# Performance work log

Hardware: AMD Instinct MI355X
Metric: run time of the kernel (lower is better)

Reference implementation:

```python
import math
import jax, jax.numpy as jnp
import numpy as np

D_MODEL = 1024
NHEAD = 16
DK = D_MODEL // NHEAD
FACTOR = 5
B, L = 4, 8192
U = max(1, min(FACTOR * math.ceil(math.log(L + 1)), L))  # 50


def setup_inputs() -> dict:
    key = jax.random.key(0)
    ks = jax.random.split(key, 10)
    s = 1.0 / math.sqrt(D_MODEL)
    inp = {
        "x": jax.random.normal(ks[0], (B, L, D_MODEL), dtype=jnp.float32),
        "Wq": jax.random.normal(ks[1], (D_MODEL, D_MODEL), dtype=jnp.float32) * s,
        "bq": jnp.zeros((D_MODEL,), dtype=jnp.float32),
        "Wk": jax.random.normal(ks[2], (D_MODEL, D_MODEL), dtype=jnp.float32) * s,
        "bk": jnp.zeros((D_MODEL,), dtype=jnp.float32),
        "Wv": jax.random.normal(ks[3], (D_MODEL, D_MODEL), dtype=jnp.float32) * s,
        "bv": jnp.zeros((D_MODEL,), dtype=jnp.float32),
        "Wo": jax.random.normal(ks[4], (D_MODEL, D_MODEL), dtype=jnp.float32) * s,
        "bo": jnp.zeros((D_MODEL,), dtype=jnp.float32),
        # randperm(L)[:U] sample of key positions (constant, like torch.randperm)
        "idx_k": jax.random.permutation(ks[5], L)[:U].astype(jnp.int32),
    }
    return inp


def reference(x, Wq, bq, Wk, bk, Wv, bv, Wo, bo, idx_k):
    Bv, Lv, _ = x.shape
    H, dk = NHEAD, DK
    u = idx_k.shape[0]
    scale = 1.0 / math.sqrt(dk)

    # projections -> [B, H, L, dk]
    Q = (x @ Wq.T + bq).reshape(Bv, Lv, H, dk).transpose(0, 2, 1, 3)
    K = (x @ Wk.T + bk).reshape(Bv, Lv, H, dk).transpose(0, 2, 1, 3)
    V = (x @ Wv.T + bv).reshape(Bv, Lv, H, dk).transpose(0, 2, 1, 3)

    # sampled scores against u random keys: [B, H, L, u]
    K_samp = K[:, :, idx_k, :]
    scores = jnp.einsum("bhld,bhud->bhlu", Q, K_samp) * scale
    M = scores.max(-1) - scores.mean(-1)                 # [B, H, L]
    _, top_idx = jax.lax.top_k(M, u)                      # [B, H, u]

    # gather selected queries and attend against ALL keys
    Q_top = jnp.take_along_axis(Q, top_idx[..., None], axis=2)   # [B, H, u, dk]
    attn = jax.nn.softmax(jnp.einsum("bhud,bhld->bhul", Q_top, K) * scale, axis=-1)
    ctx_top = jnp.einsum("bhul,bhld->bhud", attn, V)              # [B, H, u, dk]

    # mean(V) fallback, scatter selected contexts back
    ctx = jnp.broadcast_to(V.mean(axis=2, keepdims=True), (Bv, H, Lv, dk))
    bidx = jnp.arange(Bv)[:, None, None]
    hidx = jnp.arange(H)[None, :, None]
    ctx = ctx.at[bidx, hidx, top_idx].set(ctx_top)

    ctx = ctx.transpose(0, 2, 1, 3).reshape(Bv, Lv, H * dk)
    return ctx @ Wo.T + bo
```

## Files before the change

kernel.cpp:

```cpp
#include <hip/hip_runtime.h>
#include <hip/hip_bf16.h>

#define B_ 4
#define L_ 8192
#define D_ 1024
#define H_ 16
#define SCALE 0.125f
#define NC 8
#define QPAD 64
#define RS 72

typedef __attribute__((ext_vector_type(8))) short bf16x8;
typedef __attribute__((ext_vector_type(4))) float f32x4;

__device__ __forceinline__ void gl2lds16(const void* g, void* s) {
    __builtin_amdgcn_global_load_lds(
        (const __attribute__((address_space(1))) unsigned int*)g,
        (__attribute__((address_space(3))) unsigned int*)s, 16, 0, 0);
}

__device__ __forceinline__ unsigned short bfbits(float a) {
    __hip_bfloat16 h = __float2bfloat16(a);
    return *(unsigned short*)&h;
}
__device__ __forceinline__ float bf2f(unsigned short u) {
    return __uint_as_float(((unsigned)u) << 16);
}

__global__ __launch_bounds__(256) void split3_kernel(const float* __restrict__ in,
        unsigned short* __restrict__ ph, unsigned short* __restrict__ pm,
        unsigned short* __restrict__ pl, int n4) {
    int i = blockIdx.x * 256 + threadIdx.x;
    if (i >= n4) return;
    float4 v = ((const float4*)in)[i];
    float c[4] = {v.x, v.y, v.z, v.w};
    unsigned short h[4], m[4], l[4];
    #pragma unroll
    for (int j = 0; j < 4; ++j) {
        float a = c[j];
        unsigned short hb = bfbits(a);
        float rh = a - bf2f(hb);
        unsigned short mb = bfbits(rh);
        float rm = rh - bf2f(mb);
        h[j] = hb; m[j] = mb; l[j] = bfbits(rm);
    }
    ((ushort4*)ph)[i] = *(ushort4*)h;
    ((ushort4*)pm)[i] = *(ushort4*)m;
    ((ushort4*)pl)[i] = *(ushort4*)l;
}

__global__ __launch_bounds__(256) void split2_kernel(const float* __restrict__ in,
        unsigned short* __restrict__ ph, unsigned short* __restrict__ pm, int n4) {
    int i = blockIdx.x * 256 + threadIdx.x;
    if (i >= n4) return;
    float4 v = ((const float4*)in)[i];
    float c[4] = {v.x, v.y, v.z, v.w};
    unsigned short h[4], m[4];
    #pragma unroll
    for (int j = 0; j < 4; ++j) {
        float a = c[j];
        unsigned short hb = bfbits(a);
        float rh = a - bf2f(hb);
        h[j] = hb; m[j] = bfbits(rh);
    }
    ((ushort4*)ph)[i] = *(ushort4*)h;
    ((ushort4*)pm)[i] = *(ushort4*)m;
}

__global__ __launch_bounds__(256) void xmean_kernel(const float* __restrict__ x,
                                                    float* __restrict__ xmean) {
    int c = blockIdx.x;
    int j = blockIdx.y * 256 + threadIdx.x;
    int b = blockIdx.z;
    const float* xp = x + ((size_t)b * L_ + (size_t)c * 256) * D_ + j;
    float s = 0.f;
    for (int l = 0; l < 256; ++l) s += xp[(size_t)l * D_];
    atomicAdd(&xmean[b * D_ + j], s * (1.0f / L_));
}

__global__ __launch_bounds__(256) void vecmat_kernel(const float* __restrict__ in,
                                                     const float* __restrict__ W,
                                                     const float* __restrict__ bias,
                                                     float* __restrict__ out) {
    __shared__ float vs[D_];
    int b = blockIdx.y;
    int j = blockIdx.x * 256 + threadIdx.x;
    for (int t = threadIdx.x; t < D_; t += 256) vs[t] = in[b * D_ + t];
    __syncthreads();
    const float* wr = W + (size_t)j * D_;
    float acc = 0.f;
    #pragma unroll 4
    for (int k = 0; k < D_; k += 4) {
        float4 w4 = *(const float4*)(wr + k);
        acc += vs[k] * w4.x + vs[k + 1] * w4.y + vs[k + 2] * w4.z + vs[k + 3] * w4.w;
    }
    out[b * D_ + j] = acc + bias[j];
}

__global__ __launch_bounds__(256) void ksamp_kernel(const float* __restrict__ x,
                                                    const float* __restrict__ Wk,
                                                    const float* __restrict__ bk,
                                                    const int* __restrict__ idx_k,
                                                    float* __restrict__ Ksamp, int U) {
    __shared__ float vs[D_];
    int u = blockIdx.x, b = blockIdx.y;
    int row = idx_k[u];
    const float* xp = x + ((size_t)b * L_ + row) * D_;
    for (int t = threadIdx.x; t < D_; t += 256) vs[t] = xp[t];
    __syncthreads();
    #pragma unroll
    for (int r = 0; r < 4; ++r) {
        int j = r * 256 + threadIdx.x;
        const float* wr = Wk + (size_t)j * D_;
        float acc = 0.f;
        #pragma unroll 4
        for (int k = 0; k < D_; k += 4) {
            float4 w4 = *(const float4*)(wr + k);
            acc += vs[k] * w4.x + vs[k + 1] * w4.y + vs[k + 2] * w4.z + vs[k + 3] * w4.w;
        }
        Ksamp[((size_t)b * U + u) * D_ + j] = acc + bk[j];
    }
}

#define TM 128
#define TN 128
#define BK 32
#define TSZ (TM * BK)

__global__ __launch_bounds__(256) void qkv_mfma_q(
    const unsigned short* __restrict__ xh, const unsigned short* __restrict__ xm,
    const unsigned short* __restrict__ xl,
    const unsigned short* __restrict__ qh, const unsigned short* __restrict__ qm,
    const unsigned short* __restrict__ ql,
    const float* __restrict__ bq, float* __restrict__ Q) {
    __shared__ __align__(16) unsigned short As[3][TSZ];
    __shared__ __align__(16) unsigned short Bs[3][TSZ];

    const int f  = blockIdx.y * 8 + blockIdx.x;
    const int w  = (f & 7) * 256 + (f >> 3);
    const int n0 = (w & 7) * TN;
    const int m0 = (w >> 3) * TM;
    const int tid = threadIdx.x;

    const int srow = tid >> 2;
    const int scol = (tid & 3) * 8;

    const int wave = tid >> 6;
    const int lane = tid & 63;
    const int wm = (wave & 1) * 64;
    const int wn = (wave >> 1) * 64;
    const int fr = lane & 15;
    const int fk = (lane >> 4) * 8;
    const int rbase = (lane >> 4) * 4;

    f32x4 acc[4][4];
    #pragma unroll
    for (int i = 0; i < 4; ++i)
        #pragma unroll
        for (int j = 0; j < 4; ++j)
            acc[i][j] = (f32x4){0.f, 0.f, 0.f, 0.f};

    const size_t aBase = (size_t)(m0 + srow) * D_ + scol;
    const size_t bBase = (size_t)(n0 + srow) * D_ + scol;

    bf16x8 af[4], bfv[4];
    auto loadA = [&](const unsigned short* t) {
        #pragma unroll
        for (int i = 0; i < 4; ++i)
            af[i] = *(const bf16x8*)(t + (wm + i * 16 + fr) * BK + fk);
    };
    auto loadB = [&](const unsigned short* t) {
        #pragma unroll
        for (int j = 0; j < 4; ++j)
            bfv[j] = *(const bf16x8*)(t + (wn + j * 16 + fr) * BK + fk);
    };
    auto prod = [&]() {
        #pragma unroll
        for (int i = 0; i < 4; ++i)
            #pragma unroll
            for (int j = 0; j < 4; ++j)
                acc[i][j] = __builtin_amdgcn_mfma_f32_16x16x32_bf16(
                    af[i], bfv[j], acc[i][j], 0, 0, 0);
    };
    auto stage = [&](const unsigned short* g, unsigned short* s, int kt, size_t base) {
        gl2lds16(g + base + kt, s + tid * 8);
        gl2lds16(g + base + (size_t)64 * D_ + kt, s + tid * 8 + 2048);
    };

    for (int kt = 0; kt < D_; kt += BK) {
        stage(xh, &As[0][0], kt, aBase);
        stage(xm, &As[1][0], kt, aBase);
        stage(xl, &As[2][0], kt, aBase);
        stage(qh, &Bs[0][0], kt, bBase);
        stage(qm, &Bs[1][0], kt, bBase);
        stage(ql, &Bs[2][0], kt, bBase);
        __syncthreads();
        loadA(&As[0][0]); loadB(&Bs[0][0]); prod();
        loadB(&Bs[1][0]); prod();
        loadB(&Bs[2][0]); prod();
        loadA(&As[1][0]); loadB(&Bs[0][0]); prod();
        loadB(&Bs[1][0]); prod();
        loadA(&As[2][0]); loadB(&Bs[0][0]); prod();
        __syncthreads();
    }

    float biasv[4];
    #pragma unroll
    for (int j = 0; j < 4; ++j) biasv[j] = bq[n0 + wn + j * 16 + fr];

    #pragma unroll
    for (int i = 0; i < 4; ++i) {
        #pragma unroll
        for (int r = 0; r < 4; ++r) {
            size_t row = (size_t)(m0 + wm + i * 16 + rbase + r);
            #pragma unroll
            for (int j = 0; j < 4; ++j) {
                int n = n0 + wn + j * 16 + fr;
                Q[row * D_ + n] = acc[i][j][r] + biasv[j];
            }
        }
    }
}

__global__ __launch_bounds__(256) void qkv_mfma_kv(
    const unsigned short* __restrict__ xh, const unsigned short* __restrict__ xm,
    const unsigned short* __restrict__ kh, const unsigned short* __restrict__ km,
    const unsigned short* __restrict__ vh, const unsigned short* __restrict__ vm,
    const float* __restrict__ bk2, const float* __restrict__ bv,
    __hip_bfloat16* __restrict__ Kb, __hip_bfloat16* __restrict__ Vb) {
    __shared__ __align__(16) unsigned short As[2][TSZ];
    __shared__ __align__(16) unsigned short Bs[4][TSZ];

    const int f  = blockIdx.y * 8 + blockIdx.x;
    const int w  = (f & 7) * 256 + (f >> 3);
    const int n0 = (w & 7) * TN;
    const int m0 = (w >> 3) * TM;
    const int tid = threadIdx.x;

    const int srow = tid >> 2;
    const int scol = (tid & 3) * 8;

    const int wave = tid >> 6;
    const int lane = tid & 63;
    const int wm = (wave & 1) * 64;
    const int wn = (wave >> 1) * 64;
    const int fr = lane & 15;
    const int fk = (lane >> 4) * 8;
    const int rbase = (lane >> 4) * 4;

    f32x4 accK[4][4], accV[4][4];
    #pragma unroll
    for (int i = 0; i < 4; ++i)
        #pragma unroll
        for (int j = 0; j < 4; ++j) {
            accK[i][j] = (f32x4){0.f, 0.f, 0.f, 0.f};
            accV[i][j] = (f32x4){0.f, 0.f, 0.f, 0.f};
        }

    const size_t aBase = (size_t)(m0 + srow) * D_ + scol;
    const size_t bBase = (size_t)(n0 + srow) * D_ + scol;

    bf16x8 af[4], bfv[4];
    auto loadA = [&](const unsigned short* t) {
        #pragma unroll
        for (int i = 0; i < 4; ++i)
            af[i] = *(const bf16x8*)(t + (wm + i * 16 + fr) * BK + fk);
    };
    auto loadB = [&](const unsigned short* t) {
        #pragma unroll
        for (int j = 0; j < 4; ++j)
            bfv[j] = *(const bf16x8*)(t + (wn + j * 16 + fr) * BK + fk);
    };
    auto prodK = [&]() {
        #pragma unroll
        for (int i = 0; i < 4; ++i)
            #pragma unroll
            for (int j = 0; j < 4; ++j)
                accK[i][j] = __builtin_amdgcn_mfma_f32_16x16x32_bf16(
                    af[i], bfv[j], accK[i][j], 0, 0, 0);
    };
    auto prodV = [&]() {
        #pragma unroll
        for (int i = 0; i < 4; ++i)
            #pragma unroll
            for (int j = 0; j < 4; ++j)
                accV[i][j] = __builtin_amdgcn_mfma_f32_16x16x32_bf16(
                    af[i], bfv[j], accV[i][j], 0, 0, 0);
    };
    auto stage = [&](const unsigned short* g, unsigned short* s, int kt, size_t base) {
        gl2lds16(g + base + kt, s + tid * 8);
        gl2lds16(g + base + (size_t)64 * D_ + kt, s + tid * 8 + 2048);
    };

    for (int kt = 0; kt < D_; kt += BK) {
        stage(xh, &As[0][0], kt, aBase);
        stage(xm, &As[1][0], kt, aBase);
        stage(kh, &Bs[0][0], kt, bBase);
        stage(km, &Bs[1][0], kt, bBase);
        stage(vh, &Bs[2][0], kt, bBase);
        stage(vm, &Bs[3][0], kt, bBase);
        __syncthreads();
        loadA(&As[0][0]);
        loadB(&Bs[0][0]); prodK();
        loadB(&Bs[1][0]); prodK();
        loadB(&Bs[2][0]); prodV();
        loadB(&Bs[3][0]); prodV();
        loadA(&As[1][0]);
        loadB(&Bs[0][0]); prodK();
        loadB(&Bs[2][0]); prodV();
        __syncthreads();
    }

    float biasK[4], biasV[4];
    #pragma unroll
    for (int j = 0; j < 4; ++j) {
        biasK[j] = bk2[n0 + wn + j * 16 + fr];
        biasV[j] = bv[n0 + wn + j * 16 + fr];
    }

    #pragma unroll
    for (int i = 0; i < 4; ++i) {
        #pragma unroll
        for (int r = 0; r < 4; ++r) {
            size_t row = (size_t)(m0 + wm + i * 16 + rbase + r);
            #pragma unroll
            for (int j = 0; j < 4; ++j) {
                int n = n0 + wn + j * 16 + fr;
                Kb[row * D_ + n] = __float2bfloat16(accK[i][j][r] + biasK[j]);
                Vb[row * D_ + n] = __float2bfloat16(accV[i][j][r] + biasV[j]);
            }
        }
    }
}

__global__ __launch_bounds__(256) void m_kernel(const float* __restrict__ Q,
                                                const float* __restrict__ Ksamp,
                                                float* __restrict__ M, int U) {
    __shared__ float ks[64 * 64];
    int lc = blockIdx.x, h = blockIdx.y, b = blockIdx.z;
    for (int t = threadIdx.x; t < U * 64; t += 256) {
        int u = t >> 6, d = t & 63;
        ks[t] = Ksamp[((size_t)b * U + u) * D_ + h * 64 + d];
    }
    __syncthreads();
    int l = lc * 256 + threadIdx.x;
    const float* qp = Q + ((size_t)b * L_ + l) * D_ + h * 64;
    float q[64];
    #pragma unroll
    for (int i = 0; i < 16; ++i) *(float4*)&q[i * 4] = *(const float4*)(qp + i * 4);
    float mx = -INFINITY, sm = 0.f;
    for (int u = 0; u < U; ++u) {
        const float* kp = &ks[u * 64];
        float dot = 0.f;
        #pragma unroll
        for (int d = 0; d < 64; ++d) dot = fmaf(q[d], kp[d], dot);
        dot *= SCALE;
        mx = fmaxf(mx, dot);
        sm += dot;
    }
    M[((size_t)(b * H_ + h)) * L_ + l] = mx - sm / (float)U;
}

__global__ __launch_bounds__(256) void topk_kernel(const float* __restrict__ M,
                                                   int* __restrict__ topidx, int U) {
    __shared__ float vals[L_];
    __shared__ float wv[4];
    __shared__ int   wi[4];
    __shared__ int   sbest;
    int bh = blockIdx.x;
    const float* mp = M + (size_t)bh * L_;
    for (int t = threadIdx.x; t < L_; t += 256) vals[t] = mp[t];
    __syncthreads();

    float bv = -INFINITY; int bi = 0x7fffffff;
    for (int t = threadIdx.x; t < L_; t += 256) {
        float v = vals[t];
        if (v > bv || (v == bv && t < bi)) { bv = v; bi = t; }
    }
    const int lane = threadIdx.x & 63, wave = threadIdx.x >> 6;

    for (int u = 0; u < U; ++u) {
        float rv = bv; int ri = bi;
        #pragma unroll
        for (int s = 1; s < 64; s <<= 1) {
            float v2 = __shfl_xor(rv, s, 64);
            int   i2 = __shfl_xor(ri, s, 64);
            if (v2 > rv || (v2 == rv && i2 < ri)) { rv = v2; ri = i2; }
        }
        if (lane == 0) { wv[wave] = rv; wi[wave] = ri; }
        __syncthreads();
        if (threadIdx.x == 0) {
            float fv = wv[0]; int fi = wi[0];
            #pragma unroll
            for (int w = 1; w < 4; ++w) {
                if (wv[w] > fv || (wv[w] == fv && wi[w] < fi)) { fv = wv[w]; fi = wi[w]; }
            }
            topidx[bh * U + u] = fi;
            sbest = fi;
            vals[fi] = -INFINITY;
        }
        __syncthreads();
        int fi = sbest;
        if ((fi & 255) == threadIdx.x) {
            bv = -INFINITY; bi = 0x7fffffff;
            for (int t = threadIdx.x; t < L_; t += 256) {
                float v = vals[t];
                if (v > bv || (v == bv && t < bi)) { bv = v; bi = t; }
            }
        }
    }
}

__global__ __launch_bounds__(256) void attn_mfma(const float* __restrict__ Q,
        const __hip_bfloat16* __restrict__ Kb, const __hip_bfloat16* __restrict__ Vb,
        const int* __restrict__ topidx,
        float* __restrict__ part_m, float* __restrict__ part_s,
        float* __restrict__ part_acc, int U) {
    __shared__ __align__(16) unsigned short Qh[QPAD * RS];
    __shared__ __align__(16) unsigned short Qm[QPAD * RS];
    __shared__ __align__(16) unsigned short Ks[64 * RS];
    __shared__ __align__(16) unsigned short Vt[64 * RS];
    __shared__ __align__(16) unsigned short Ph[QPAD * RS];

    const int c = blockIdx.x, h = blockIdx.y, b = blockIdx.z;
    const int bh = b * H_ + h;
    const int tid = threadIdx.x;
    const int wave = tid >> 6, lane = tid & 63;
    const int w16 = wave * 16;
    const int fr = lane & 15;
    const int quad = lane >> 4;
    const int fk = quad * 8;
    const int l0 = c * (L_ / NC);

    {
        int u = tid >> 2;
        int d0 = (tid & 3) * 16;
        unsigned short hbuf[16], mbuf[16];
        if (u < U) {
            int row = topidx[bh * U + u];
            const float* qp = Q + ((size_t)b * L_ + row) * D_ + h * 64 + d0;
            #pragma unroll
            for (int i = 0; i < 16; ++i) {
                float v = qp[i] * SCALE;
                unsigned short hb = bfbits(v);
                hbuf[i] = hb;
                mbuf[i] = bfbits(v - bf2f(hb));
            }
        } else {
            #pragma unroll
            for (int i = 0; i < 16; ++i) { hbuf[i] = 0; mbuf[i] = 0; }
        }
        #pragma unroll
        for (int i = 0; i < 2; ++i) {
            *(uint4*)&Qh[u * RS + d0 + i * 8] = ((uint4*)hbuf)[i];
            *(uint4*)&Qm[u * RS + d0 + i * 8] = ((uint4*)mbuf)[i];
        }
    }

    float m_r[4], s_r[4];
    f32x4 acc_o[4];
    #pragma unroll
    for (int r = 0; r < 4; ++r) { m_r[r] = -INFINITY; s_r[r] = 0.f; }
    #pragma unroll
    for (int n = 0; n < 4; ++n) acc_o[n] = (f32x4){0.f, 0.f, 0.f, 0.f};

    __syncthreads();

    for (int kt = 0; kt < L_ / NC; kt += 64) {
        {
            int key = tid >> 3;
            int d0 = (tid & 7) * 8;
            const __hip_bfloat16* kp = Kb + ((size_t)b * L_ + l0 + kt) * D_ + h * 64;
            *(uint4*)&Ks[key * RS + d0] = *(const uint4*)(kp + (size_t)key * D_ + d0);
            *(uint4*)&Ks[(key + 32) * RS + d0] =
                *(const uint4*)(kp + (size_t)(key + 32) * D_ + d0);
        }
        {
            int key = tid >> 2;
            int d0 = (tid & 3) * 16;
            const __hip_bfloat16* vp =
                Vb + ((size_t)b * L_ + l0 + kt + key) * D_ + h * 64 + d0;
            unsigned short vbuf[16];
            *(uint4*)&vbuf[0] = *(const uint4*)(vp);
            *(uint4*)&vbuf[8] = *(const uint4*)(vp + 8);
            #pragma unroll
            for (int i = 0; i < 16; ++i) Vt[(d0 + i) * RS + key] = vbuf[i];
        }
        __syncthreads();

        f32x4 sacc[4];
        #pragma unroll
        for (int n = 0; n < 4; ++n) {
            sacc[n] = (f32x4){0.f, 0.f, 0.f, 0.f};
            #pragma unroll
            for (int ks = 0; ks < 2; ++ks) {
                int k0 = ks * 32;
                bf16x8 ah = *(const bf16x8*)&Qh[(w16 + fr) * RS + k0 + fk];
                bf16x8 am = *(const bf16x8*)&Qm[(w16 + fr) * RS + k0 + fk];
                bf16x8 bb = *(const bf16x8*)&Ks[(n * 16 + fr) * RS + k0 + fk];
                sacc[n] = __builtin_amdgcn_mfma_f32_16x16x32_bf16(ah, bb, sacc[n], 0, 0, 0);
                sacc[n] = __builtin_amdgcn_mfma_f32_16x16x32_bf16(am, bb, sacc[n], 0, 0, 0);
            }
        }

        float p[4][4];
        #pragma unroll
        for (int r = 0; r < 4; ++r) {
            float rowmax = fmaxf(fmaxf(sacc[0][r], sacc[1][r]),
                                 fmaxf(sacc[2][r], sacc[3][r]));
            #pragma unroll
            for (int msk = 1; msk <= 8; msk <<= 1)
                rowmax = fmaxf(rowmax, __shfl_xor(rowmax, msk, 64));
            float mnew = fmaxf(m_r[r], rowmax);
            float alpha = __expf(m_r[r] - mnew);
            float rowsum = 0.f;
            #pragma unroll
            for (int n = 0; n < 4; ++n) {
                p[n][r] = __expf(sacc[n][r] - mnew);
                rowsum += p[n][r];
            }
            #pragma unroll
            for (int msk = 1; msk <= 8; msk <<= 1)
                rowsum += __shfl_xor(rowsum, msk, 64);
            s_r[r] = s_r[r] * alpha + rowsum;
            m_r[r] = mnew;
            #pragma unroll
            for (int n = 0; n < 4; ++n) acc_o[n][r] *= alpha;
        }

        #pragma unroll
        for (int r = 0; r < 4; ++r)
            #pragma unroll
            for (int n = 0; n < 4; ++n)
                Ph[(w16 + quad * 4 + r) * RS + n * 16 + fr] = bfbits(p[n][r]);

        #pragma unroll
        for (int n = 0; n < 4; ++n) {
            #pragma unroll
            for (int ks = 0; ks < 2; ++ks) {
                int k0 = ks * 32;
                bf16x8 pa = *(const bf16x8*)&Ph[(w16 + fr) * RS + k0 + fk];
                bf16x8 vb = *(const bf16x8*)&Vt[(n * 16 + fr) * RS + k0 + fk];
                acc_o[n] = __builtin_amdgcn_mfma_f32_16x16x32_bf16(pa, vb, acc_o[n], 0, 0, 0);
            }
        }
        __syncthreads();
    }

    #pragma unroll
    for (int r = 0; r < 4; ++r) {
        int q = w16 + quad * 4 + r;
        if (q < U) {
            size_t base = ((size_t)(bh * QPAD + q)) * NC + c;
            if (fr == 0) { part_m[base] = m_r[r]; part_s[base] = s_r[r]; }
            #pragma unroll
            for (int n = 0; n < 4; ++n)
                part_acc[base * 64 + n * 16 + fr] = acc_o[n][r];
        }
    }
}

__global__ __launch_bounds__(64) void attn_combine(const float* __restrict__ part_m,
        const float* __restrict__ part_s, const float* __restrict__ part_acc,
        float* __restrict__ ctx_top, int U) {
    int u = blockIdx.x, h = blockIdx.y, b = blockIdx.z;
    int bh = b * H_ + h;
    int d = threadIdx.x;
    size_t base = ((size_t)(bh * QPAD + u)) * NC;
    float M = -INFINITY;
    #pragma unroll
    for (int c = 0; c < NC; ++c) M = fmaxf(M, part_m[base + c]);
    float S = 0.f, A = 0.f;
    #pragma unroll
    for (int c = 0; c < NC; ++c) {
        float f = __expf(part_m[base + c] - M);
        S += part_s[base + c] * f;
        A += part_acc[(base + c) * 64 + d] * f;
    }
    ctx_top[(((size_t)bh) * U + u) * 64 + d] = A / S;
}

__global__ __launch_bounds__(256) void fill_base_kernel(const float* __restrict__ base,
                                                        float* __restrict__ out) {
    size_t i = (size_t)blockIdx.x * 256 + threadIdx.x;
    int col4 = (int)(i & 255);
    int b = (int)(i >> 21);
    ((float4*)out)[i] = ((const float4*)base)[b * 256 + col4];
}

__global__ __launch_bounds__(256) void delta_kernel(const float* __restrict__ ctx_top,
        const float* __restrict__ vmean, const float* __restrict__ Wo,
        const int* __restrict__ topidx, float* __restrict__ out, int U) {
    __shared__ float cd[64];
    int u = blockIdx.x, h = blockIdx.y, b = blockIdx.z;
    int row = topidx[(b * H_ + h) * U + u];
    if (threadIdx.x < 64) {
        cd[threadIdx.x] = ctx_top[(((size_t)(b * H_ + h)) * U + u) * 64 + threadIdx.x]
                        - vmean[b * D_ + h * 64 + threadIdx.x];
    }
    __syncthreads();
    float* op = out + ((size_t)b * L_ + row) * D_;
    #pragma unroll
    for (int r = 0; r < 4; ++r) {
        int j = r * 256 + threadIdx.x;
        const float* wr = Wo + (size_t)j * D_ + h * 64;
        float dlt = 0.f;
        #pragma unroll
        for (int k = 0; k < 64; k += 4) {
            float4 w4 = *(const float4*)(wr + k);
            dlt += cd[k] * w4.x + cd[k + 1] * w4.y + cd[k + 2] * w4.z + cd[k + 3] * w4.w;
        }
        atomicAdd(op + j, dlt);
    }
}

extern "C" void kernel_launch(void* const* d_in, const int* in_sizes, int n_in,
                              void* d_out, int out_size, void* d_ws, size_t ws_size,
                              hipStream_t stream) {
    const float* x   = (const float*)d_in[0];
    const float* Wq  = (const float*)d_in[1];
    const float* bq  = (const float*)d_in[2];
    const float* Wk  = (const float*)d_in[3];
    const float* bk  = (const float*)d_in[4];
    const float* Wv  = (const float*)d_in[5];
    const float* bv  = (const float*)d_in[6];
    const float* Wo  = (const float*)d_in[7];
    const float* bo  = (const float*)d_in[8];
    const int* idx_k = (const int*)d_in[9];
    const int U = in_sizes[9];
    float* out = (float*)d_out;
    (void)n_in; (void)ws_size;

    char* ws = (char*)d_ws;
    size_t off = 0;
    auto alloc = [&](size_t bytes) -> void* {
        void* p = ws + off;
        off += (bytes + 255) & ~(size_t)255;
        return p;
    };
    float* Q              = (float*)alloc((size_t)B_ * L_ * D_ * 4);
    __hip_bfloat16* Kb    = (__hip_bfloat16*)alloc((size_t)B_ * L_ * D_ * 2);
    __hip_bfloat16* Vb    = (__hip_bfloat16*)alloc((size_t)B_ * L_ * D_ * 2);
    unsigned short* xh    = (unsigned short*)alloc((size_t)B_ * L_ * D_ * 2);
    unsigned short* xm    = (unsigned short*)alloc((size_t)B_ * L_ * D_ * 2);
    unsigned short* xl    = (unsigned short*)alloc((size_t)B_ * L_ * D_ * 2);
    unsigned short* wqh   = (unsigned short*)alloc((size_t)D_ * D_ * 2);
    unsigned short* wqm   = (unsigned short*)alloc((size_t)D_ * D_ * 2);
    unsigned short* wql   = (unsigned short*)alloc((size_t)D_ * D_ * 2);
    unsigned short* wkh   = (unsigned short*)alloc((size_t)D_ * D_ * 2);
    unsigned short* wkm   = (unsigned short*)alloc((size_t)D_ * D_ * 2);
    unsigned short* wvh   = (unsigned short*)alloc((size_t)D_ * D_ * 2);
    unsigned short* wvm   = (unsigned short*)alloc((size_t)D_ * D_ * 2);
    float* Ksamp          = (float*)alloc((size_t)B_ * 64 * D_ * 4);
    float* Mbuf           = (float*)alloc((size_t)B_ * H_ * L_ * 4);
    int*   topidx         = (int*)alloc((size_t)B_ * H_ * 64 * 4);
    float* xmean          = (float*)alloc((size_t)B_ * D_ * 4);
    float* vmean          = (float*)alloc((size_t)B_ * D_ * 4);
    float* base           = (float*)alloc((size_t)B_ * D_ * 4);
    float* ctxt           = (float*)alloc((size_t)B_ * H_ * 64 * 64 * 4);
    float* part_m         = (float*)alloc((size_t)B_ * H_ * QPAD * NC * 4);
    float* part_s         = (float*)alloc((size_t)B_ * H_ * QPAD * NC * 4);
    float* part_acc       = (float*)alloc((size_t)B_ * H_ * QPAD * NC * 64 * 4);

    hipMemsetAsync(xmean, 0, (size_t)B_ * D_ * 4, stream);
    xmean_kernel<<<dim3(32, 4, B_), 256, 0, stream>>>(x, xmean);
    vecmat_kernel<<<dim3(4, B_), 256, 0, stream>>>(xmean, Wv, bv, vmean);
    vecmat_kernel<<<dim3(4, B_), 256, 0, stream>>>(vmean, Wo, bo, base);
    ksamp_kernel<<<dim3(U, B_), 256, 0, stream>>>(x, Wk, bk, idx_k, Ksamp, U);

    const int n4x = B_ * L_ * D_ / 4;
    const int n4w = D_ * D_ / 4;
    split3_kernel<<<dim3(n4x / 256), 256, 0, stream>>>(x, xh, xm, xl, n4x);
    split3_kernel<<<dim3(n4w / 256), 256, 0, stream>>>(Wq, wqh, wqm, wql, n4w);
    split2_kernel<<<dim3(n4w / 256), 256, 0, stream>>>(Wk, wkh, wkm, n4w);
    split2_kernel<<<dim3(n4w / 256), 256, 0, stream>>>(Wv, wvm ? wvh : wvh, wvm, n4w);

    qkv_mfma_kv<<<dim3(8, 256), 256, 0, stream>>>(xh, xm, wkh, wkm, wvh, wvm,
                                                  bk, bv, Kb, Vb);
    qkv_mfma_q<<<dim3(8, 256), 256, 0, stream>>>(xh, xm, xl, wqh, wqm, wql,
                                                 bq, Q);

    m_kernel<<<dim3(32, H_, B_), 256, 0, stream>>>(Q, Ksamp, Mbuf, U);
    topk_kernel<<<dim3(B_ * H_), 256, 0, stream>>>(Mbuf, topidx, U);
    attn_mfma<<<dim3(NC, H_, B_), 256, 0, stream>>>(Q, Kb, Vb, topidx,
                                                    part_m, part_s, part_acc, U);
    attn_combine<<<dim3(U, H_, B_), 64, 0, stream>>>(part_m, part_s, part_acc, ctxt, U);
    fill_base_kernel<<<dim3(out_size / 4 / 256), 256, 0, stream>>>(base, out);
    delta_kernel<<<dim3(U, H_, B_), 256, 0, stream>>>(ctxt, vmean, Wo, topidx, out, U);
}
```

Before: 1.867 ms.

## Split K/V projection into separate blocks with double-buffered LDS staging

The fused K+V projection kernel is split so each block computes either K or V, which doubles the grid and halves the per-thread accumulator registers. The main loop now double-buffers LDS, so the next k-tile is staged while MFMAs run on the current one. Both projection kernels also drop the swizzled block-index remap in favour of a direct blockIdx mapping. In exchange, the x tiles are now loaded twice, once by the K blocks and once by the V blocks, and L2 locality may change without the remap.

```diff
diff --git a/kernel.cpp b/kernel.cpp
--- a/kernel.cpp
+++ b/kernel.cpp
@@ -127,7 +127,7 @@
 #define BK 32
 #define TSZ (TM * BK)
 
-__global__ __launch_bounds__(256) void qkv_mfma_q(
+__global__ __launch_bounds__(256) void qkv_q(
     const unsigned short* __restrict__ xh, const unsigned short* __restrict__ xm,
     const unsigned short* __restrict__ xl,
     const unsigned short* __restrict__ qh, const unsigned short* __restrict__ qm,
@@ -136,10 +136,8 @@
     __shared__ __align__(16) unsigned short As[3][TSZ];
     __shared__ __align__(16) unsigned short Bs[3][TSZ];
 
-    const int f  = blockIdx.y * 8 + blockIdx.x;
-    const int w  = (f & 7) * 256 + (f >> 3);
-    const int n0 = (w & 7) * TN;
-    const int m0 = (w >> 3) * TM;
+    const int n0 = blockIdx.x * TN;
+    const int m0 = blockIdx.y * TM;
     const int tid = threadIdx.x;
 
     const int srow = tid >> 2;
@@ -222,20 +220,24 @@
     }
 }
 
-__global__ __launch_bounds__(256) void qkv_mfma_kv(
+__global__ __launch_bounds__(256) void qkv_kv(
     const unsigned short* __restrict__ xh, const unsigned short* __restrict__ xm,
     const unsigned short* __restrict__ kh, const unsigned short* __restrict__ km,
     const unsigned short* __restrict__ vh, const unsigned short* __restrict__ vm,
     const float* __restrict__ bk2, const float* __restrict__ bv,
     __hip_bfloat16* __restrict__ Kb, __hip_bfloat16* __restrict__ Vb) {
-    __shared__ __align__(16) unsigned short As[2][TSZ];
-    __shared__ __align__(16) unsigned short Bs[4][TSZ];
-
-    const int f  = blockIdx.y * 8 + blockIdx.x;
-    const int w  = (f & 7) * 256 + (f >> 3);
-    const int n0 = (w & 7) * TN;
-    const int m0 = (w >> 3) * TM;
-    const int tid = threadIdx.x;
+    __shared__ __align__(16) unsigned short As[2][2][TSZ];
+    __shared__ __align__(16) unsigned short Bs[2][2][TSZ];
+
+    const int which = blockIdx.x >> 3;
+    const int nb    = (blockIdx.x & 7) * TN;
+    const int m0    = blockIdx.y * TM;
+    const int tid   = threadIdx.x;
+
+    const unsigned short* Bh = which ? vh : kh;
+    const unsigned short* Bm = which ? vm : km;
+    const float* bias        = which ? bv : bk2;
+    __hip_bfloat16* Out      = which ? Vb : Kb;
 
     const int srow = tid >> 2;
     const int scol = (tid & 3) * 8;
@@ -248,17 +250,15 @@
     const int fk = (lane >> 4) * 8;
     const int rbase = (lane >> 4) * 4;
 
-    f32x4 accK[4][4], accV[4][4];
+    f32x4 acc[4][4];
     #pragma unroll
     for (int i = 0; i < 4; ++i)
         #pragma unroll
-        for (int j = 0; j < 4; ++j) {
-            accK[i][j] = (f32x4){0.f, 0.f, 0.f, 0.f};
-            accV[i][j] = (f32x4){0.f, 0.f, 0.f, 0.f};
-        }
+        for (int j = 0; j < 4; ++j)
+            acc[i][j] = (f32x4){0.f, 0.f, 0.f, 0.f};
 
     const size_t aBase = (size_t)(m0 + srow) * D_ + scol;
-    const size_t bBase = (size_t)(n0 + srow) * D_ + scol;
+    const size_t bBase = (size_t)(nb + srow) * D_ + scol;
 
     bf16x8 af[4], bfv[4];
     auto loadA = [&](const unsigned short* t) {
@@ -271,52 +271,43 @@
         for (int j = 0; j < 4; ++j)
             bfv[j] = *(const bf16x8*)(t + (wn + j * 16 + fr) * BK + fk);
     };
-    auto prodK = [&]() {
+    auto prod = [&]() {
         #pragma unroll
         for (int i = 0; i < 4; ++i)
             #pragma unroll
             for (int j = 0; j < 4; ++j)
-                accK[i][j] = __builtin_amdgcn_mfma_f32_16x16x32_bf16(
-                    af[i], bfv[j], accK[i][j], 0, 0, 0);
-    };
-    auto prodV = [&]() {
-        #pragma unroll
-        for (int i = 0; i < 4; ++i)
-            #pragma unroll
-            for (int j = 0; j < 4; ++j)
-                accV[i][j] = __builtin_amdgcn_mfma_f32_16x16x32_bf16(
-                    af[i], bfv[j], accV[i][j], 0, 0, 0);
-    };
-    auto stage = [&](const unsigned short* g, unsigned short* s, int kt, size_t base) {
-        gl2lds16(g + base + kt, s + tid * 8);
-        gl2lds16(g + base + (size_t)64 * D_ + kt, s + tid * 8 + 2048);
-    };
-
-    for (int kt = 0; kt < D_; kt += BK) {
-        stage(xh, &As[0][0], kt, aBase);
-        stage(xm, &As[1][0], kt, aBase);
-        stage(kh, &Bs[0][0], kt, bBase);
-        stage(km, &Bs[1][0], kt, bBase);
-        stage(vh, &Bs[2][0], kt, bBase);
-        stage(vm, &Bs[3][0], kt, bBase);
+                acc[i][j] = __builtin_amdgcn_mfma_f32_16x16x32_bf16(
+                    af[i], bfv[j], acc[i][j], 0, 0, 0);
+    };
+    auto stage = [&](int buf, int kt) {
+        gl2lds16(xh + aBase + kt, &As[buf][0][tid * 8]);
+        gl2lds16(xh + aBase + (size_t)64 * D_ + kt, &As[buf][0][tid * 8 + 2048]);
+        gl2lds16(xm + aBase + kt, &As[buf][1][tid * 8]);
+        gl2lds16(xm + aBase + (size_t)64 * D_ + kt, &As[buf][1][tid * 8 + 2048]);
+        gl2lds16(Bh + bBase + kt, &Bs[buf][0][tid * 8]);
+        gl2lds16(Bh + bBase + (size_t)64 * D_ + kt, &Bs[buf][0][tid * 8 + 2048]);
+        gl2lds16(Bm + bBase + kt, &Bs[buf][1][tid * 8]);
+        gl2lds16(Bm + bBase + (size_t)64 * D_ + kt, &Bs[buf][1][tid * 8 + 2048]);
+    };
+
+    stage(0, 0);
+    __syncthreads();
+
+    const int NKT = D_ / BK;
+    for (int t = 0; t < NKT; ++t) {
+        const int cur = t & 1;
+        if (t + 1 < NKT) stage(cur ^ 1, (t + 1) * BK);
+        loadA(&As[cur][0][0]);
+        loadB(&Bs[cur][0][0]); prod();
+        loadB(&Bs[cur][1][0]); prod();
+        loadA(&As[cur][1][0]);
+        loadB(&Bs[cur][0][0]); prod();
         __syncthreads();
-        loadA(&As[0][0]);
-        loadB(&Bs[0][0]); prodK();
-        loadB(&Bs[1][0]); prodK();
-        loadB(&Bs[2][0]); prodV();
-        loadB(&Bs[3][0]); prodV();
-        loadA(&As[1][0]);
-        loadB(&Bs[0][0]); prodK();
-        loadB(&Bs[2][0]); prodV();
-        __syncthreads();
-    }
-
-    float biasK[4], biasV[4];
-    #pragma unroll
-    for (int j = 0; j < 4; ++j) {
-        biasK[j] = bk2[n0 + wn + j * 16 + fr];
-        biasV[j] = bv[n0 + wn + j * 16 + fr];
-    }
+    }
+
+    float biasv[4];
+    #pragma unroll
+    for (int j = 0; j < 4; ++j) biasv[j] = bias[nb + wn + j * 16 + fr];
 
     #pragma unroll
     for (int i = 0; i < 4; ++i) {
@@ -325,9 +316,8 @@
             size_t row = (size_t)(m0 + wm + i * 16 + rbase + r);
             #pragma unroll
             for (int j = 0; j < 4; ++j) {
-                int n = n0 + wn + j * 16 + fr;
-                Kb[row * D_ + n] = __float2bfloat16(accK[i][j][r] + biasK[j]);
-                Vb[row * D_ + n] = __float2bfloat16(accV[i][j][r] + biasV[j]);
+                int n = nb + wn + j * 16 + fr;
+                Out[row * D_ + n] = __float2bfloat16(acc[i][j][r] + biasv[j]);
             }
         }
     }
@@ -673,12 +663,11 @@
     split3_kernel<<<dim3(n4x / 256), 256, 0, stream>>>(x, xh, xm, xl, n4x);
     split3_kernel<<<dim3(n4w / 256), 256, 0, stream>>>(Wq, wqh, wqm, wql, n4w);
     split2_kernel<<<dim3(n4w / 256), 256, 0, stream>>>(Wk, wkh, wkm, n4w);
-    split2_kernel<<<dim3(n4w / 256), 256, 0, stream>>>(Wv, wvm ? wvh : wvh, wvm, n4w);
-
-    qkv_mfma_kv<<<dim3(8, 256), 256, 0, stream>>>(xh, xm, wkh, wkm, wvh, wvm,
-                                                  bk, bv, Kb, Vb);
-    qkv_mfma_q<<<dim3(8, 256), 256, 0, stream>>>(xh, xm, xl, wqh, wqm, wql,
-                                                 bq, Q);
+    split2_kernel<<<dim3(n4w / 256), 256, 0, stream>>>(Wv, wvh, wvm, n4w);
+
+    qkv_q<<<dim3(8, 256), 256, 0, stream>>>(xh, xm, xl, wqh, wqm, wql, bq, Q);
+    qkv_kv<<<dim3(16, 256), 256, 0, stream>>>(xh, xm, wkh, wkm, wvh, wvm,
+                                              bk, bv, Kb, Vb);
 
     m_kernel<<<dim3(32, H_, B_), 256, 0, stream>>>(Q, Ksamp, Mbuf, U);
     topk_kernel<<<dim3(B_ * H_), 256, 0, stream>>>(Mbuf, topidx, U);
```

After: 1.807 ms. 1.03x faster.
